# Kernel tuning notes

Hardware: AMD Instinct MI355X
Metric: run time of the kernel (lower is better)

Reference implementation:

```python
import jax, jax.numpy as jnp
import numpy as np

D_MODEL = 1024
N_HEAD = 16
HEAD_DIM = D_MODEL // N_HEAD
SCALING = HEAD_DIM ** -0.5
EPS = 1e-6


def setup_inputs() -> dict:
    key = jax.random.key(0)
    ks = jax.random.split(key, 12)
    B, LQ, LK = 4, 2048, 2048
    s = (D_MODEL ** -0.5)
    return {
        "querys": jax.random.normal(ks[0], (B, LQ, D_MODEL), jnp.float32),
        "keys": jax.random.normal(ks[1], (B, LK, D_MODEL), jnp.float32),
        "values": jax.random.normal(ks[2], (B, LK, D_MODEL), jnp.float32),
        "key_mask": jnp.zeros((B, LK), dtype=bool),
        "Wq": jax.random.normal(ks[3], (D_MODEL, D_MODEL), jnp.float32) * s,
        "bq": jnp.zeros((D_MODEL,), jnp.float32),
        "Wk": jax.random.normal(ks[4], (D_MODEL, D_MODEL), jnp.float32) * s,
        "bk": jnp.zeros((D_MODEL,), jnp.float32),
        "Wv": jax.random.normal(ks[5], (D_MODEL, D_MODEL), jnp.float32) * s,
        "bv": jnp.zeros((D_MODEL,), jnp.float32),
        "Wo": jax.random.normal(ks[6], (D_MODEL, D_MODEL), jnp.float32) * s,
        "bo": jnp.zeros((D_MODEL,), jnp.float32),
    }


def _feature_map(x):
    # elu_feature_map: elu(x) + 1
    return jax.nn.elu(x) + 1.0


def reference(querys, keys, values, key_mask, Wq, bq, Wk, bk, Wv, bv, Wo, bo):
    B, Lq, _ = querys.shape
    Lk = keys.shape[1]
    q = (querys @ Wq.T + bq) * SCALING
    k = keys @ Wk.T + bk
    v = values @ Wv.T + bv
    Q = _feature_map(q.reshape(B, Lq, N_HEAD, HEAD_DIM))  # bqnd
    K = _feature_map(k.reshape(B, Lk, N_HEAD, HEAD_DIM))  # bsnd
    K = jnp.where(key_mask[:, :, None, None], 0.0, K)
    V = v.reshape(B, Lk, N_HEAD, HEAD_DIM)                 # bsnm
    # State computed once (info reused for every query step in the torch loop)
    S = jnp.einsum('bsnd,bsnm->bnmd', K, V)               # [B,H,Dv,Dk]
    Z = K.sum(axis=1)                                     # [B,H,Dk]
    QZ = 1.0 / (jnp.einsum('bqnd,bnd->bqn', Q, Z) + EPS)  # [B,Lq,H]
    out = jnp.einsum('bqnd,bnmd,bqn->bqnm', Q, S, QZ)     # [B,Lq,H,Dv]
    out = out.reshape(B, Lq, D_MODEL)
    return out @ Wo.T + bo
```

## Files before the change

### kernel.cpp

```cpp
#include <hip/hip_runtime.h>
#include <cstdint>
#include <cstddef>


typedef __attribute__((ext_vector_type(8))) short short8;
typedef __attribute__((ext_vector_type(4))) float f32x4;

#define EPS_F 1e-6f

__device__ __forceinline__ float bf2f(short u) {
  union { unsigned int i; float f; } c;
  c.i = ((unsigned int)(unsigned short)u) << 16;
  return c.f;
}
__device__ __forceinline__ unsigned short f2bf(float f) {
  union { float f; unsigned int i; } c;
  c.f = f;
  return (unsigned short)((c.i + 0x7fffu + ((c.i >> 16) & 1u)) >> 16);
}

typedef __attribute__((address_space(1))) const unsigned int gu32;
typedef __attribute__((address_space(3))) unsigned int lu32;

__device__ __forceinline__ void gload_lds16(const void* g, void* l) {
  __builtin_amdgcn_global_load_lds((gu32*)g, (lu32*)l, 16, 0, 0);
}

__device__ __forceinline__ void gemm_mainloop(const char* Ab, const char* Bb,
                                              char* AsB, char* BsB,
                                              int tm, int tn, f32x4 acc[4][4]) {
  const int t = threadIdx.x;
  const int l = t & 63;
  const int w = t >> 6;
  const int srow = l >> 3, sslot = l & 7;
  const int sso16 = ((sslot ^ srow) << 4);
  const int rd0 = ((l & 15) << 7) | ((((l >> 4) + 0) ^ (l & 7)) << 4);
  const int rd1 = ((l & 15) << 7) | ((((l >> 4) + 4) ^ (l & 7)) << 4);
  const int wr = (w >> 1) << 6;
  const int wc = (w & 1) << 6;

#pragma unroll
  for (int i = 0; i < 4; ++i)
#pragma unroll
    for (int j = 0; j < 4; ++j) acc[i][j] = f32x4{0.f, 0.f, 0.f, 0.f};

  const char* Ag = Ab + (size_t)tm * 2048;
  const char* Bg = Bb + (size_t)tn * 2048;

  for (int kt = 0; kt < 16; ++kt) {
    __syncthreads();
    const int kofs = kt << 7;
#pragma unroll
    for (int i = 0; i < 4; ++i) {
      const int rr = (((w << 2) + i) << 3) + srow;
      gload_lds16(Ag + (size_t)rr * 2048 + kofs + sso16,
                  AsB + rr * 128 + (sslot << 4));
      gload_lds16(Bg + (size_t)rr * 2048 + kofs + sso16,
                  BsB + rr * 128 + (sslot << 4));
    }
    __syncthreads();
#pragma unroll
    for (int kk = 0; kk < 2; ++kk) {
      const int rdo = kk ? rd1 : rd0;
      short8 a[4], b[4];
#pragma unroll
      for (int i = 0; i < 4; ++i)
        a[i] = *(const short8*)(AsB + ((wr + i * 16) << 7) + rdo);
#pragma unroll
      for (int j = 0; j < 4; ++j)
        b[j] = *(const short8*)(BsB + ((wc + j * 16) << 7) + rdo);
#pragma unroll
      for (int i = 0; i < 4; ++i)
#pragma unroll
        for (int j = 0; j < 4; ++j)
          acc[i][j] = __builtin_amdgcn_mfma_f32_16x16x32_bf16(a[i], b[j],
                                                              acc[i][j], 0, 0, 0);
    }
  }
}

__global__ __launch_bounds__(256) void proj_gemm(
    const short* __restrict__ qb, const short* __restrict__ kb,
    const short* __restrict__ vb, const short* __restrict__ Wq,
    const short* __restrict__ Wk, const short* __restrict__ Wv,
    const float* __restrict__ bq, const float* __restrict__ bk,
    const float* __restrict__ bv, unsigned short* __restrict__ Qf,
    unsigned short* __restrict__ Kf, unsigned short* __restrict__ Vf,
    const unsigned char* __restrict__ mask) {
  __shared__ char As[16384], Bs[16384];
  const int mode = blockIdx.z;
  const short* A = mode == 0 ? qb : (mode == 1 ? kb : vb);
  const short* B = mode == 0 ? Wq : (mode == 1 ? Wk : Wv);
  const float* bias = mode == 0 ? bq : (mode == 1 ? bk : bv);
  unsigned short* O = mode == 0 ? Qf : (mode == 1 ? Kf : Vf);
  const int tm = blockIdx.x << 7, tn = blockIdx.y << 7;
  f32x4 acc[4][4];
  gemm_mainloop((const char*)A, (const char*)B, As, Bs, tm, tn, acc);

  const int l = threadIdx.x & 63, w = threadIdx.x >> 6;
  const int wr = (w >> 1) << 6, wc = (w & 1) << 6;
  const int lr = (l >> 4) << 2, lc = l & 15;
#pragma unroll
  for (int i = 0; i < 4; ++i) {
#pragma unroll
    for (int r = 0; r < 4; ++r) {
      const int row = tm + wr + i * 16 + lr + r;
      const bool msk = (mode == 1) && (mask[row] != 0);
      const int b = row >> 11, s = row & 2047;
#pragma unroll
      for (int j = 0; j < 4; ++j) {
        const int col = tn + wc + j * 16 + lc;
        float v = acc[i][j][r] + bias[col];
        if (mode == 0) {
          v *= 0.125f;
          v = (v > 0.f) ? (v + 1.f) : __expf(v);
        } else if (mode == 1) {
          v = (v > 0.f) ? (v + 1.f) : __expf(v);
          if (msk) v = 0.f;
        }
        const int h = col >> 6, d = col & 63;
        O[((size_t)(b * 16 + h) * 2048 + s) * 64 + d] = f2bf(v);
      }
    }
  }
}

__global__ __launch_bounds__(256) void final_gemm(const short* __restrict__ A,
                                                  const short* __restrict__ Wo,
                                                  const float* __restrict__ bo,
                                                  float* __restrict__ out) {
  __shared__ char As[16384], Bs[16384];
  const int tm = blockIdx.x << 7, tn = blockIdx.y << 7;
  f32x4 acc[4][4];
  gemm_mainloop((const char*)A, (const char*)Wo, As, Bs, tm, tn, acc);
  const int l = threadIdx.x & 63, w = threadIdx.x >> 6;
  const int wr = (w >> 1) << 6, wc = (w & 1) << 6;
  const int lr = (l >> 4) << 2, lc = l & 15;
#pragma unroll
  for (int i = 0; i < 4; ++i)
#pragma unroll
    for (int r = 0; r < 4; ++r) {
      const int row = tm + wr + i * 16 + lr + r;
#pragma unroll
      for (int j = 0; j < 4; ++j) {
        const int col = tn + wc + j * 16 + lc;
        out[(size_t)row * 1024 + col] = acc[i][j][r] + bo[col];
      }
    }
}

__global__ __launch_bounds__(256) void s_state(
    const unsigned short* __restrict__ Kf, const unsigned short* __restrict__ Vf,
    unsigned short* __restrict__ Sext) {
  __shared__ char sh[65536];
  unsigned short* Ks = (unsigned short*)sh;
  unsigned short* Vs = (unsigned short*)(sh + 32768);
  float* red = (float*)sh;
  const int bh = blockIdx.x;
  const int t = threadIdx.x, l = t & 63, w = t >> 6;
  const unsigned short* Kb = Kf + (size_t)bh * 131072;
  const unsigned short* Vb = Vf + (size_t)bh * 131072;

  f32x4 acc[5][4];
#pragma unroll
  for (int i = 0; i < 5; ++i)
#pragma unroll
    for (int j = 0; j < 4; ++j) acc[i][j] = f32x4{0.f, 0.f, 0.f, 0.f};

  const short onebf = ((l & 15) == 0) ? (short)0x3F80 : (short)0;
  short8 a4;
#pragma unroll
  for (int e = 0; e < 8; ++e) a4[e] = onebf;

  for (int ch = 0; ch < 8; ++ch) {
    __syncthreads();
    const size_t gb = (size_t)ch * 16384;
#pragma unroll
    for (int i = 0; i < 8; ++i) {
      const int eo = (i * 256 + t) * 8;
      gload_lds16(Kb + gb + eo, (char*)Ks + (size_t)eo * 2);
      gload_lds16(Vb + gb + eo, (char*)Vs + (size_t)eo * 2);
    }
    __syncthreads();
#pragma unroll
    for (int st = 0; st < 2; ++st) {
      const int sb = (w << 6) + (st << 5) + ((l >> 4) << 3);
      short8 b[4], a[4];
#pragma unroll
      for (int dj = 0; dj < 4; ++dj)
#pragma unroll
        for (int e = 0; e < 8; ++e)
          b[dj][e] = (short)Ks[(sb + e) * 64 + dj * 16 + (l & 15)];
#pragma unroll
      for (int mi = 0; mi < 4; ++mi)
#pragma unroll
        for (int e = 0; e < 8; ++e)
          a[mi][e] = (short)Vs[(sb + e) * 64 + mi * 16 + (l & 15)];
#pragma unroll
      for (int mi = 0; mi < 4; ++mi)
#pragma unroll
        for (int dj = 0; dj < 4; ++dj)
          acc[mi][dj] = __builtin_amdgcn_mfma_f32_16x16x32_bf16(
              a[mi], b[dj], acc[mi][dj], 0, 0, 0);
#pragma unroll
      for (int dj = 0; dj < 4; ++dj)
        acc[4][dj] = __builtin_amdgcn_mfma_f32_16x16x32_bf16(
            a4, b[dj], acc[4][dj], 0, 0, 0);
    }
  }

  __syncthreads();
  const int lr = (l >> 4) << 2, lc = l & 15;
  for (int wv = 0; wv < 4; ++wv) {
    if (w == wv) {
#pragma unroll
      for (int mi = 0; mi < 5; ++mi)
#pragma unroll
        for (int dj = 0; dj < 4; ++dj)
#pragma unroll
          for (int r = 0; r < 4; ++r) {
            const int idx = (mi * 16 + lr + r) * 64 + dj * 16 + lc;
            if (wv == 0) red[idx] = acc[mi][dj][r];
            else         red[idx] += acc[mi][dj][r];
          }
    }
    __syncthreads();
  }
  unsigned short* So = Sext + (size_t)bh * 5120;
#pragma unroll
  for (int i = 0; i < 20; ++i) So[i * 256 + t] = f2bf(red[i * 256 + t]);
}

__global__ __launch_bounds__(256) void out_gemm(const unsigned short* __restrict__ Qf,
                                                const unsigned short* __restrict__ Sext,
                                                unsigned short* __restrict__ out2) {
  __shared__ char Qs[16384], Ss[10240];
  const int qt = blockIdx.x, bh = blockIdx.y;
  const int t = threadIdx.x, l = t & 63, w = t >> 6;
  const int srow = l >> 3, sslot = l & 7;
  const int sso16 = ((sslot ^ srow) << 4);
  const char* Qg = (const char*)(Qf + ((size_t)bh * 2048 + qt * 128) * 64);
  const char* Sg = (const char*)(Sext + (size_t)bh * 5120);
  for (int i = w; i < 16; i += 4) {
    const int rr = (i << 3) + srow;
    gload_lds16(Qg + (size_t)rr * 128 + sso16, Qs + rr * 128 + (sslot << 4));
  }
  for (int i = w; i < 10; i += 4) {
    const int rr = (i << 3) + srow;
    gload_lds16(Sg + (size_t)rr * 128 + sso16, Ss + rr * 128 + (sslot << 4));
  }
  __syncthreads();
  const int rd0 = ((l & 15) << 7) | ((((l >> 4) + 0) ^ (l & 7)) << 4);
  const int rd1 = ((l & 15) << 7) | ((((l >> 4) + 4) ^ (l & 7)) << 4);
  f32x4 acc[2][5];
#pragma unroll
  for (int i = 0; i < 2; ++i)
#pragma unroll
    for (int j = 0; j < 5; ++j) acc[i][j] = f32x4{0.f, 0.f, 0.f, 0.f};
#pragma unroll
  for (int kk = 0; kk < 2; ++kk) {
    const int rdo = kk ? rd1 : rd0;
    short8 a[2], b[5];
#pragma unroll
    for (int i = 0; i < 2; ++i)
      a[i] = *(const short8*)(Qs + ((w * 32 + i * 16) << 7) + rdo);
#pragma unroll
    for (int j = 0; j < 5; ++j)
      b[j] = *(const short8*)(Ss + ((j * 16) << 7) + rdo);
#pragma unroll
    for (int i = 0; i < 2; ++i)
#pragma unroll
      for (int j = 0; j < 5; ++j)
        acc[i][j] = __builtin_amdgcn_mfma_f32_16x16x32_bf16(a[i], b[j],
                                                            acc[i][j], 0, 0, 0);
  }
  const int b_ = bh >> 4, h = bh & 15;
#pragma unroll
  for (int i = 0; i < 2; ++i) {
#pragma unroll
    for (int r = 0; r < 4; ++r) {
      const float dv = __shfl(acc[i][4][r], (l & 48));
      const float qz = 1.f / (dv + EPS_F);
      const int q = qt * 128 + w * 32 + i * 16 + ((l >> 4) << 2) + r;
      unsigned short* po = out2 + ((size_t)b_ * 2048 + q) * 1024 + h * 64;
#pragma unroll
      for (int j = 0; j < 4; ++j) po[j * 16 + (l & 15)] = f2bf(acc[i][j][r] * qz);
    }
  }
}

__global__ __launch_bounds__(256) void convert_all(
    const float* __restrict__ s0, const float* __restrict__ s1,
    const float* __restrict__ s2, const float* __restrict__ s3,
    const float* __restrict__ s4, const float* __restrict__ s5,
    const float* __restrict__ s6, unsigned short* __restrict__ d0,
    unsigned short* __restrict__ d1, unsigned short* __restrict__ d2,
    unsigned short* __restrict__ d3, unsigned short* __restrict__ d4,
    unsigned short* __restrict__ d5, unsigned short* __restrict__ d6) {
  const int x = blockIdx.x;
  int seg, blk;
  if (x < 12288) { seg = x >> 12; blk = x & 4095; }
  else           { seg = 3 + ((x - 12288) >> 9); blk = (x - 12288) & 511; }
  const float* src;
  unsigned short* dst;
  switch (seg) {
    case 0: src = s0; dst = d0; break;
    case 1: src = s1; dst = d1; break;
    case 2: src = s2; dst = d2; break;
    case 3: src = s3; dst = d3; break;
    case 4: src = s4; dst = d4; break;
    case 5: src = s5; dst = d5; break;
    default: src = s6; dst = d6; break;
  }
  const int idx = (blk * 256 + threadIdx.x) * 8;
  const f32x4 a = *(const f32x4*)(src + idx);
  const f32x4 b = *(const f32x4*)(src + idx + 4);
  union { unsigned short u[8]; short8 v; } o;
#pragma unroll
  for (int e = 0; e < 4; ++e) {
    o.u[e] = f2bf(a[e]);
    o.u[4 + e] = f2bf(b[e]);
  }
  *(short8*)(dst + idx) = o.v;
}

extern "C" void kernel_launch(void* const* d_in, const int* in_sizes, int n_in,
                              void* d_out, int out_size, void* d_ws,
                              size_t ws_size, hipStream_t stream) {
  const float* querys = (const float*)d_in[0];
  const float* keys = (const float*)d_in[1];
  const float* values = (const float*)d_in[2];
  const unsigned char* mask = (const unsigned char*)d_in[3];
  const float* Wq = (const float*)d_in[4];
  const float* bq = (const float*)d_in[5];
  const float* Wk = (const float*)d_in[6];
  const float* bk = (const float*)d_in[7];
  const float* Wv = (const float*)d_in[8];
  const float* bv = (const float*)d_in[9];
  const float* Wo = (const float*)d_in[10];
  const float* bo = (const float*)d_in[11];
  float* out = (float*)d_out;

  char* ws = (char*)d_ws;
  unsigned short* qb  = (unsigned short*)(ws + 0);
  unsigned short* kb  = (unsigned short*)(ws + 16777216);
  unsigned short* vb  = (unsigned short*)(ws + 33554432);
  unsigned short* wqb = (unsigned short*)(ws + 50331648);
  unsigned short* wkb = (unsigned short*)(ws + 52428800);
  unsigned short* wvb = (unsigned short*)(ws + 54525952);
  unsigned short* wob = (unsigned short*)(ws + 56623104);
  unsigned short* Qf  = (unsigned short*)(ws + 58720256);
  unsigned short* Kf  = (unsigned short*)(ws + 75497472);
  unsigned short* Vf  = (unsigned short*)(ws + 92274688);
  unsigned short* Sx  = (unsigned short*)(ws + 16777216);
  unsigned short* out2 = qb;

  convert_all<<<dim3(14336), 256, 0, stream>>>(querys, keys, values, Wq, Wk,
                                               Wv, Wo, qb, kb, vb, wqb, wkb,
                                               wvb, wob);
  proj_gemm<<<dim3(64, 8, 3), 256, 0, stream>>>(
      (const short*)qb, (const short*)kb, (const short*)vb, (const short*)wqb,
      (const short*)wkb, (const short*)wvb, bq, bk, bv, Qf, Kf, Vf, mask);
  s_state<<<dim3(64), 256, 0, stream>>>(Kf, Vf, Sx);
  out_gemm<<<dim3(16, 64), 256, 0, stream>>>(Qf, Sx, out2);
  final_gemm<<<dim3(64, 8), 256, 0, stream>>>((const short*)out2,
                                              (const short*)wob, bo, out);
}
```

Measured before the change: 292.3 us.

## Double-buffer LDS tiles in GEMM mainloop to overlap loads with MFMA

The shared GEMM mainloop now uses two LDS buffers per operand. It issues the global-to-LDS load for the next K tile before computing the current one, and uses vmcnt waits plus raw s_barrier in place of the two __syncthreads per iteration. The aim is to hide global load latency behind MFMA work in both the projection and output GEMMs. LDS use per block doubles to 64KB, which may reduce occupancy, and the hand-counted vmcnt depends on each thread issuing exactly eight loads per stage.

```diff
diff --git a/kernel.cpp b/kernel.cpp
--- a/kernel.cpp
+++ b/kernel.cpp
@@ -26,8 +26,23 @@
   __builtin_amdgcn_global_load_lds((gu32*)g, (lu32*)l, 16, 0, 0);
 }
 
+__device__ __forceinline__ void stage_tile(const char* Ag, const char* Bg,
+                                           char* As, char* Bs, int kofs,
+                                           int w, int srow, int sslot,
+                                           int sso16) {
+#pragma unroll
+  for (int i = 0; i < 4; ++i) {
+    const int rr = (((w << 2) + i) << 3) + srow;
+    gload_lds16(Ag + (size_t)rr * 2048 + kofs + sso16,
+                As + rr * 128 + (sslot << 4));
+    gload_lds16(Bg + (size_t)rr * 2048 + kofs + sso16,
+                Bs + rr * 128 + (sslot << 4));
+  }
+}
+
 __device__ __forceinline__ void gemm_mainloop(const char* Ab, const char* Bb,
-                                              char* AsB, char* BsB,
+                                              char* As0, char* Bs0,
+                                              char* As1, char* Bs1,
                                               int tm, int tn, f32x4 acc[4][4]) {
   const int t = threadIdx.x;
   const int l = t & 63;
@@ -47,28 +62,31 @@
   const char* Ag = Ab + (size_t)tm * 2048;
   const char* Bg = Bb + (size_t)tn * 2048;
 
+  stage_tile(Ag, Bg, As0, Bs0, 0, w, srow, sslot, sso16);
+
   for (int kt = 0; kt < 16; ++kt) {
-    __syncthreads();
-    const int kofs = kt << 7;
-#pragma unroll
-    for (int i = 0; i < 4; ++i) {
-      const int rr = (((w << 2) + i) << 3) + srow;
-      gload_lds16(Ag + (size_t)rr * 2048 + kofs + sso16,
-                  AsB + rr * 128 + (sslot << 4));
-      gload_lds16(Bg + (size_t)rr * 2048 + kofs + sso16,
-                  BsB + rr * 128 + (sslot << 4));
-    }
-    __syncthreads();
+    char* Ac = (kt & 1) ? As1 : As0;
+    char* Bc = (kt & 1) ? Bs1 : Bs0;
+    if (kt < 15) {
+      char* An = (kt & 1) ? As0 : As1;
+      char* Bn = (kt & 1) ? Bs0 : Bs1;
+      stage_tile(Ag, Bg, An, Bn, (kt + 1) << 7, w, srow, sslot, sso16);
+      asm volatile("s_waitcnt vmcnt(8)" ::: "memory");
+    } else {
+      asm volatile("s_waitcnt vmcnt(0)" ::: "memory");
+    }
+    __builtin_amdgcn_s_barrier();
+    asm volatile("" ::: "memory");
 #pragma unroll
     for (int kk = 0; kk < 2; ++kk) {
       const int rdo = kk ? rd1 : rd0;
       short8 a[4], b[4];
 #pragma unroll
       for (int i = 0; i < 4; ++i)
-        a[i] = *(const short8*)(AsB + ((wr + i * 16) << 7) + rdo);
+        a[i] = *(const short8*)(Ac + ((wr + i * 16) << 7) + rdo);
 #pragma unroll
       for (int j = 0; j < 4; ++j)
-        b[j] = *(const short8*)(BsB + ((wc + j * 16) << 7) + rdo);
+        b[j] = *(const short8*)(Bc + ((wc + j * 16) << 7) + rdo);
 #pragma unroll
       for (int i = 0; i < 4; ++i)
 #pragma unroll
@@ -76,6 +94,8 @@
           acc[i][j] = __builtin_amdgcn_mfma_f32_16x16x32_bf16(a[i], b[j],
                                                               acc[i][j], 0, 0, 0);
     }
+    asm volatile("" ::: "memory");
+    __builtin_amdgcn_s_barrier();
   }
 }
 
@@ -87,7 +107,7 @@
     const float* __restrict__ bv, unsigned short* __restrict__ Qf,
     unsigned short* __restrict__ Kf, unsigned short* __restrict__ Vf,
     const unsigned char* __restrict__ mask) {
-  __shared__ char As[16384], Bs[16384];
+  __shared__ char As[2][16384], Bs[2][16384];
   const int mode = blockIdx.z;
   const short* A = mode == 0 ? qb : (mode == 1 ? kb : vb);
   const short* B = mode == 0 ? Wq : (mode == 1 ? Wk : Wv);
@@ -95,7 +115,8 @@
   unsigned short* O = mode == 0 ? Qf : (mode == 1 ? Kf : Vf);
   const int tm = blockIdx.x << 7, tn = blockIdx.y << 7;
   f32x4 acc[4][4];
-  gemm_mainloop((const char*)A, (const char*)B, As, Bs, tm, tn, acc);
+  gemm_mainloop((const char*)A, (const char*)B, As[0], Bs[0], As[1], Bs[1],
+                tm, tn, acc);
 
   const int l = threadIdx.x & 63, w = threadIdx.x >> 6;
   const int wr = (w >> 1) << 6, wc = (w & 1) << 6;
@@ -129,10 +150,11 @@
                                                   const short* __restrict__ Wo,
                                                   const float* __restrict__ bo,
                                                   float* __restrict__ out) {
-  __shared__ char As[16384], Bs[16384];
+  __shared__ char As[2][16384], Bs[2][16384];
   const int tm = blockIdx.x << 7, tn = blockIdx.y << 7;
   f32x4 acc[4][4];
-  gemm_mainloop((const char*)A, (const char*)Wo, As, Bs, tm, tn, acc);
+  gemm_mainloop((const char*)A, (const char*)Wo, As[0], Bs[0], As[1], Bs[1],
+                tm, tn, acc);
   const int l = threadIdx.x & 63, w = threadIdx.x >> 6;
   const int wr = (w >> 1) << 6, wc = (w & 1) << 6;
   const int lr = (l >> 4) << 2, lc = l & 15;
```

Result: no change. 292.3 us (+0.0%).
